# Kernel optimization log

Hardware: AMD Instinct MI355X
Metric: run time of the kernel (lower is better)

## Reference

```python
import jax, jax.numpy as jnp
import numpy as np
from jax import lax

DN = ('NCHW', 'OIHW', 'NCHW')


def setup_inputs() -> dict:
    key = jax.random.key(0)
    ks = jax.random.split(key, 5)
    B, C, H, W = 1, 128, 64, 64
    heads = 4
    return {
        'x_q': jax.random.normal(ks[0], (B, C, H, W), jnp.float32),
        'x_kv': jax.random.normal(ks[1], (B, C, H, W), jnp.float32),
        'w_qkv': jax.random.normal(ks[2], (3 * C, C, 1, 1), jnp.float32) * 0.05,
        'w_dw': jax.random.normal(ks[3], (3 * C, 1, 3, 3), jnp.float32) * 0.2,
        'w_proj': jax.random.normal(ks[4], (C, C, 1, 1), jnp.float32) * 0.05,
        'temperature': jnp.ones((heads, 1, 1), jnp.float32),
    }


def reference(x_q, x_kv, w_qkv, w_dw, w_proj, temperature):
    B, C, H, W = x_q.shape
    heads = temperature.shape[0]
    hd = C // heads
    N = H * W

    # shared qkv 1x1 conv + depthwise 3x3 conv on concatenated [2B,C,H,W]
    x = jnp.concatenate([x_q, x_kv], axis=0)
    qkv = lax.conv_general_dilated(x, w_qkv, (1, 1), 'VALID', dimension_numbers=DN)
    qkv = lax.conv_general_dilated(qkv, w_dw, (1, 1), 'SAME',
                                   feature_group_count=3 * C, dimension_numbers=DN)
    q, k, v = jnp.split(qkv, 3, axis=1)
    q = q[:B]          # query branch from x_q
    k = k[B:]          # key/value branch from x_kv
    v = v[B:]

    def to_heads(t):   # [B,C,H,W] -> [B,h,N,d]
        return t.reshape(B, heads, hd, N).transpose(0, 1, 3, 2)

    attn = jnp.einsum('bhnd,bhmd->bhnm', to_heads(q), to_heads(k)) * temperature
    attn = jax.nn.softmax(attn, axis=-1)
    out = jnp.einsum('bhnm,bhmd->bhnd', attn, to_heads(v))
    out = out.transpose(0, 1, 3, 2).reshape(B, C, H, W)
    return lax.conv_general_dilated(out, w_proj, (1, 1), 'VALID', dimension_numbers=DN)
```

## Files before the change

kernel.cpp:

```cpp
#include <hip/hip_runtime.h>

typedef short bf16x4 __attribute__((ext_vector_type(4)));
typedef short bf16x8 __attribute__((ext_vector_type(8)));
typedef float f32x4 __attribute__((ext_vector_type(4)));
typedef unsigned short u16x4 __attribute__((ext_vector_type(4)));
typedef unsigned short u16x8 __attribute__((ext_vector_type(8)));

__device__ __forceinline__ unsigned short f2bf(float f) {
  union { float f; unsigned u; } v; v.f = f;
  unsigned r = v.u + 0x7FFFu + ((v.u >> 16) & 1u);
  return (unsigned short)(r >> 16);
}
__device__ __forceinline__ unsigned fbits(float f) {
  union { float f; unsigned u; } x; x.f = f; return x.u;
}
__device__ __forceinline__ float bfloat(unsigned u) {
  union { unsigned u; float f; } x; x.u = u; return x.f;
}
__device__ __forceinline__ float fexp2(float x) {
#if __has_builtin(__builtin_amdgcn_exp2f)
  return __builtin_amdgcn_exp2f(x);
#else
  return exp2f(x);
#endif
}
__device__ __forceinline__ f32x4 pv_mfma(bf16x4 a, bf16x4 b, f32x4 c) {
#if __has_builtin(__builtin_amdgcn_mfma_f32_16x16x16bf16_1k)
  return __builtin_amdgcn_mfma_f32_16x16x16bf16_1k(a, b, c, 0, 0, 0);
#else
  bf16x8 az = {a[0], a[1], a[2], a[3], 0, 0, 0, 0};
  bf16x8 bz = {b[0], b[1], b[2], b[3], 0, 0, 0, 0};
  return __builtin_amdgcn_mfma_f32_16x16x32_bf16(az, bz, c, 0, 0, 0);
#endif
}

__global__ __launch_bounds__(256)
void cast_kernel(const float* __restrict__ Xq, const float* __restrict__ Xkv,
                 const float* __restrict__ Wqkv, const float* __restrict__ Wproj,
                 unsigned short* __restrict__ XT, unsigned short* __restrict__ Wq16,
                 unsigned short* __restrict__ Wph, unsigned short* __restrict__ Wpl)
{
  const int b = blockIdx.x, t = threadIdx.x;
  if (b < 256) {
    __shared__ __align__(16) float Tl[64][68];
    const int img = b >> 7, kt = (b >> 6) & 1, nt = b & 63;
    const float* X = img ? Xkv : Xq;
    #pragma unroll
    for (int i = 0; i < 4; ++i) {
      int e = i * 256 + t;
      int r = e >> 4, c4 = (e & 15) * 4;
      *(f32x4*)&Tl[r][c4] = *(const f32x4*)&X[(kt * 64 + r) * 4096 + nt * 64 + c4];
    }
    __syncthreads();
    unsigned short* out = XT + img * (4096 * 128);
    #pragma unroll
    for (int i = 0; i < 2; ++i) {
      int u = i * 256 + t;
      int n = u >> 3, kg = u & 7;
      u16x8 tv;
      #pragma unroll
      for (int j = 0; j < 8; ++j) tv[j] = f2bf(Tl[kg * 8 + j][n]);
      *(u16x8*)&out[(nt * 64 + n) * 128 + kt * 64 + kg * 8] = tv;
    }
  } else {
    const int wb = b - 256;
    if (wb < 3) {
      #pragma unroll 4
      for (int i = 0; i < 64; ++i) {
        int idx = wb * 16384 + i * 256 + t;
        Wq16[idx] = f2bf(Wqkv[idx]);
      }
    } else {
      #pragma unroll 4
      for (int i = 0; i < 64; ++i) {
        int idx = i * 256 + t;
        float v = Wproj[idx];
        unsigned short h = f2bf(v);
        float hf = bfloat((unsigned)h << 16);
        Wph[idx] = h;
        Wpl[idx] = f2bf(v - hf);
      }
    }
  }
}

__global__ __launch_bounds__(256)
void gemm_qkv_kernel(const unsigned short* __restrict__ XT,
                     const unsigned short* __restrict__ Wq16,
                     unsigned short* __restrict__ Y16)
{
  const int t = threadIdx.x;
  const int w = t >> 6, c = t & 15, g = (t & 63) >> 4;
  const int n0 = blockIdx.x * 32;
  const int ob = blockIdx.y;
  const int o_base = ob * 64 + w * 16;
  const unsigned short* B = XT + (ob >= 2 ? 4096 * 128 : 0);
  f32x4 acc0 = {0.f, 0.f, 0.f, 0.f}, acc1 = {0.f, 0.f, 0.f, 0.f};
  #pragma unroll
  for (int ks = 0; ks < 4; ++ks) {
    bf16x8 a = *(const bf16x8*)&Wq16[(o_base + c) * 128 + ks * 32 + g * 8];
    bf16x8 b0 = *(const bf16x8*)&B[(n0 + c) * 128 + ks * 32 + g * 8];
    bf16x8 b1 = *(const bf16x8*)&B[(n0 + 16 + c) * 128 + ks * 32 + g * 8];
    acc0 = __builtin_amdgcn_mfma_f32_16x16x32_bf16(a, b0, acc0, 0, 0, 0);
    acc1 = __builtin_amdgcn_mfma_f32_16x16x32_bf16(a, b1, acc1, 0, 0, 0);
  }
  #pragma unroll
  for (int i = 0; i < 4; ++i) {
    Y16[(o_base + 4 * g + i) * 4096 + n0 + c] = f2bf(acc0[i]);
    Y16[(o_base + 4 * g + i) * 4096 + n0 + 16 + c] = f2bf(acc1[i]);
  }
}

__global__ __launch_bounds__(256)
void gemm_proj_kernel(const unsigned short* __restrict__ Oth,
                      const unsigned short* __restrict__ Otl,
                      const unsigned short* __restrict__ Wph,
                      const unsigned short* __restrict__ Wpl, float* __restrict__ Y)
{
  const int t = threadIdx.x;
  const int w = t >> 6, c = t & 15, g = (t & 63) >> 4;
  const int n0 = blockIdx.x * 32;
  const int o_base = blockIdx.y * 64 + w * 16;
  f32x4 acc0 = {0.f, 0.f, 0.f, 0.f}, acc1 = {0.f, 0.f, 0.f, 0.f};
  #pragma unroll
  for (int ks = 0; ks < 4; ++ks) {
    const int ko = ks * 32 + g * 8;
    bf16x8 ah = *(const bf16x8*)&Wph[(o_base + c) * 128 + ko];
    bf16x8 al = *(const bf16x8*)&Wpl[(o_base + c) * 128 + ko];
    bf16x8 bh0 = *(const bf16x8*)&Oth[(n0 + c) * 128 + ko];
    bf16x8 bl0 = *(const bf16x8*)&Otl[(n0 + c) * 128 + ko];
    bf16x8 bh1 = *(const bf16x8*)&Oth[(n0 + 16 + c) * 128 + ko];
    bf16x8 bl1 = *(const bf16x8*)&Otl[(n0 + 16 + c) * 128 + ko];
    acc0 = __builtin_amdgcn_mfma_f32_16x16x32_bf16(al, bh0, acc0, 0, 0, 0);
    acc0 = __builtin_amdgcn_mfma_f32_16x16x32_bf16(ah, bl0, acc0, 0, 0, 0);
    acc0 = __builtin_amdgcn_mfma_f32_16x16x32_bf16(ah, bh0, acc0, 0, 0, 0);
    acc1 = __builtin_amdgcn_mfma_f32_16x16x32_bf16(al, bh1, acc1, 0, 0, 0);
    acc1 = __builtin_amdgcn_mfma_f32_16x16x32_bf16(ah, bl1, acc1, 0, 0, 0);
    acc1 = __builtin_amdgcn_mfma_f32_16x16x32_bf16(ah, bh1, acc1, 0, 0, 0);
  }
  #pragma unroll
  for (int i = 0; i < 4; ++i) {
    Y[(o_base + 4 * g + i) * 4096 + n0 + c] = acc0[i];
    Y[(o_base + 4 * g + i) * 4096 + n0 + 16 + c] = acc1[i];
  }
}

__global__ __launch_bounds__(256)
void dwconv_kernel(const unsigned short* __restrict__ T16, const float* __restrict__ Wd,
                   const float* __restrict__ temp, unsigned short* __restrict__ Qt,
                   unsigned short* __restrict__ Kt, unsigned short* __restrict__ Vb)
{
  __shared__ __align__(16) float P[4096];
  const int jc = blockIdx.x;
  const int t = threadIdx.x;
  const unsigned short* in = T16 + jc * 4096;
  #pragma unroll
  for (int i = 0; i < 2; ++i) {
    u16x8 v = *(const u16x8*)&in[(i * 256 + t) * 8];
    #pragma unroll
    for (int j = 0; j < 8; ++j)
      P[(i * 256 + t) * 8 + j] = bfloat((unsigned)v[j] << 16);
  }
  float w[9];
  #pragma unroll
  for (int k = 0; k < 9; ++k) w[k] = Wd[jc * 9 + k];
  const float scale = (jc < 128) ? temp[jc >> 5] * 1.4426950408889634f : 1.0f;
  __syncthreads();

  const int hh = (jc >> 5) & 3, dd = jc & 31;
  unsigned short* outT = (jc < 128 ? Qt : Kt) + (hh * 4096) * 32 + dd;
  unsigned short* outV = Vb + (jc - 256) * 4096;
  const bool is_v = (jc >= 256);

  #pragma unroll 4
  for (int i = 0; i < 16; ++i) {
    int idx = i * 256 + t;
    int y = idx >> 6, x = idx & 63;
    float acc = 0.f;
    #pragma unroll
    for (int dy = -1; dy <= 1; ++dy) {
      int yy = y + dy;
      if (yy < 0 || yy > 63) continue;
      #pragma unroll
      for (int dx = -1; dx <= 1; ++dx) {
        int xx = x + dx;
        if (xx < 0 || xx > 63) continue;
        acc += w[(dy + 1) * 3 + (dx + 1)] * P[yy * 64 + xx];
      }
    }
    unsigned short r = f2bf(acc * scale);
    if (is_v) outV[idx] = r;
    else      outT[idx * 32] = r;
  }
}

__global__ __launch_bounds__(1024, 4)
void attn_kernel(const unsigned short* __restrict__ Qt,
                 const unsigned short* __restrict__ Kt,
                 const unsigned short* __restrict__ Vb,
                 unsigned short* __restrict__ Oth, unsigned short* __restrict__ Otl)
{
  __shared__ __align__(16) char lds[40960];
  const int t = threadIdx.x;
  const int wv = t >> 6;
  const int g4 = wv >> 2, qw = wv & 3;
  const int l = t & 63;
  const int c = l & 15, g = l >> 4;
  const int h = blockIdx.y;
  const int nq = blockIdx.x * 64;
  const int m0w = wv * 256;

  bf16x8 qf[4];
  #pragma unroll
  for (int s = 0; s < 4; ++s)
    qf[s] = *(const bf16x8*)&Qt[(h * 4096 + nq + s * 16 + c) * 32 + g * 8];

  f32x4 oh[4][2];
  #pragma unroll
  for (int s = 0; s < 4; ++s) {
    oh[s][0] = (f32x4){0.f, 0.f, 0.f, 0.f};
    oh[s][1] = (f32x4){0.f, 0.f, 0.f, 0.f};
  }
  float lsum[4] = {0.f, 0.f, 0.f, 0.f};

  const unsigned short* Kb  = Kt + (h * 4096 + m0w + c) * 32 + g * 8;
  const unsigned short* Vb0 = Vb + (h * 32 + c) * 4096 + m0w + g * 4;
  const unsigned short* Vb1 = Vb0 + 16 * 4096;

  #pragma unroll 4
  for (int j = 0; j < 16; ++j) {
    bf16x8 kf = *(const bf16x8*)&Kb[j * 512];
    bf16x4 vf0 = *(const bf16x4*)&Vb0[j * 16];
    bf16x4 vf1 = *(const bf16x4*)&Vb1[j * 16];
    #pragma unroll
    for (int s = 0; s < 4; ++s) {
      f32x4 z = {0.f, 0.f, 0.f, 0.f};
      f32x4 sv = __builtin_amdgcn_mfma_f32_16x16x32_bf16(kf, qf[s], z, 0, 0, 0);
      float e0 = fexp2(sv[0]);
      float e1 = fexp2(sv[1]);
      float e2 = fexp2(sv[2]);
      float e3 = fexp2(sv[3]);
      lsum[s] += (e0 + e1) + (e2 + e3);
      union { unsigned u[2]; bf16x4 v; } pu;
      pu.u[0] = __builtin_amdgcn_perm(fbits(e1), fbits(e0), 0x07060302);
      pu.u[1] = __builtin_amdgcn_perm(fbits(e3), fbits(e2), 0x07060302);
      oh[s][0] = pv_mfma(vf0, pu.v, oh[s][0]);
      oh[s][1] = pv_mfma(vf1, pu.v, oh[s][1]);
    }
  }

  #pragma unroll
  for (int s = 0; s < 4; ++s) {
    lsum[s] += __shfl_xor(lsum[s], 16, 64);
    lsum[s] += __shfl_xor(lsum[s], 32, 64);
  }

  __syncthreads();
  float* OG  = (float*)lds;
  float* lfq = (float*)(lds + 34048);
  float* lf  = (float*)(lds + 36864);
  if (l < 16) {
    #pragma unroll
    for (int s = 0; s < 4; ++s)
      lf[(g4 * 4 + qw) * 64 + s * 16 + c] = lsum[s];
  }
  for (int r = 0; r < 4; ++r) {
    if (qw == r) {
      #pragma unroll
      for (int s = 0; s < 4; ++s)
        #pragma unroll
        for (int i = 0; i < 4; ++i) {
          int d0 = 4 * g + i;
          float* p0 = &OG[g4 * 2112 + d0 * 66 + s * 16 + c];
          float* p1 = &OG[g4 * 2112 + (16 + d0) * 66 + s * 16 + c];
          if (r == 0) { *p0 = oh[s][0][i];  *p1 = oh[s][1][i]; }
          else        { *p0 += oh[s][0][i]; *p1 += oh[s][1][i]; }
        }
    }
    __syncthreads();
  }
  if (t < 64) {
    float a = 0.f;
    #pragma unroll
    for (int ww = 0; ww < 16; ++ww) a += lf[ww * 64 + t];
    lfq[t] = a;
  }
  __syncthreads();

  #pragma unroll
  for (int e = t; e < 2048; e += 1024) {
    int d = e & 31, q = e >> 5;
    float s4 = OG[0 * 2112 + d * 66 + q] + OG[1 * 2112 + d * 66 + q] +
               OG[2 * 2112 + d * 66 + q] + OG[3 * 2112 + d * 66 + q];
    float val = s4 / lfq[q];
    unsigned short hi = f2bf(val);
    float hf = bfloat((unsigned)hi << 16);
    int idx = (blockIdx.x * 64 + q) * 128 + h * 32 + d;
    Oth[idx] = hi;
    Otl[idx] = f2bf(val - hf);
  }
}

extern "C" void kernel_launch(void* const* d_in, const int* in_sizes, int n_in,
                              void* d_out, int out_size, void* d_ws, size_t ws_size,
                              hipStream_t stream) {
  const float* xq    = (const float*)d_in[0];
  const float* xkv   = (const float*)d_in[1];
  const float* wqkv  = (const float*)d_in[2];
  const float* wdw   = (const float*)d_in[3];
  const float* wproj = (const float*)d_in[4];
  const float* temp  = (const float*)d_in[5];
  float* out = (float*)d_out;

  char* ws = (char*)d_ws;
  unsigned short* t16  = (unsigned short*)ws;
  unsigned short* xt   = (unsigned short*)(ws + 3145728);
  unsigned short* wq16 = (unsigned short*)(ws + 5242880);
  unsigned short* wph  = (unsigned short*)(ws + 5341184);
  unsigned short* wpl  = (unsigned short*)(ws + 5373952);
  unsigned short* qt   = (unsigned short*)(ws + 5406720);
  unsigned short* kt   = (unsigned short*)(ws + 6455296);
  unsigned short* vb   = (unsigned short*)(ws + 7503872);
  unsigned short* oth  = (unsigned short*)(ws + 8552448);
  unsigned short* otl  = (unsigned short*)(ws + 9601024);

  cast_kernel<<<dim3(260), 256, 0, stream>>>(xq, xkv, wqkv, wproj, xt, wq16, wph, wpl);
  gemm_qkv_kernel<<<dim3(128, 6), 256, 0, stream>>>(xt, wq16, t16);
  dwconv_kernel<<<dim3(384), 256, 0, stream>>>(t16, wdw, temp, qt, kt, vb);
  attn_kernel<<<dim3(64, 4), 1024, 0, stream>>>(qt, kt, vb, oth, otl);
  gemm_proj_kernel<<<dim3(128, 2), 256, 0, stream>>>(oth, otl, wph, wpl, out);
}
```

Measured before the change: 57.38 us.

## Fuse input casting into GEMMs, split dwconv rows, use LDS atomics in attention

Removes the separate cast kernel. The QKV GEMM now reads fp32 inputs and weights directly, transposes through LDS and converts with packed bf16 instructions, while the projection GEMM splits its weights into hi/lo parts on the fly. The depthwise conv is split into four row-quarter blocks per channel with halo loads, which gives more blocks and less LDS each. The attention epilogue replaces the serialized four-round reduction with LDS atomic adds into a single buffer, cutting shared memory and barriers. In exchange it adds redundant weight conversion per block and possible atomic contention in LDS.

Result: slower. 90.80 us (+58.2%).

```diff
diff --git a/kernel.cpp b/kernel.cpp
--- a/kernel.cpp
+++ b/kernel.cpp
@@ -23,6 +23,11 @@
 #else
   return exp2f(x);
 #endif
+}
+__device__ __forceinline__ unsigned cvt_pk_bf16(float a, float b) {
+  unsigned r;
+  asm("v_cvt_pk_bf16_f32 %0, %1, %2" : "=v"(r) : "v"(a), "v"(b));
+  return r;
 }
 __device__ __forceinline__ f32x4 pv_mfma(bf16x4 a, bf16x4 b, f32x4 c) {
 #if __has_builtin(__builtin_amdgcn_mfma_f32_16x16x16bf16_1k)
@@ -35,114 +40,69 @@
 }
 
 __global__ __launch_bounds__(256)
-void cast_kernel(const float* __restrict__ Xq, const float* __restrict__ Xkv,
-                 const float* __restrict__ Wqkv, const float* __restrict__ Wproj,
-                 unsigned short* __restrict__ XT, unsigned short* __restrict__ Wq16,
-                 unsigned short* __restrict__ Wph, unsigned short* __restrict__ Wpl)
+void qkvT_kernel(const float* __restrict__ Xq, const float* __restrict__ Xkv,
+                 const float* __restrict__ Wqkv, unsigned short* __restrict__ Y16)
 {
-  const int b = blockIdx.x, t = threadIdx.x;
-  if (b < 256) {
-    __shared__ __align__(16) float Tl[64][68];
-    const int img = b >> 7, kt = (b >> 6) & 1, nt = b & 63;
-    const float* X = img ? Xkv : Xq;
-    #pragma unroll
-    for (int i = 0; i < 4; ++i) {
-      int e = i * 256 + t;
-      int r = e >> 4, c4 = (e & 15) * 4;
-      *(f32x4*)&Tl[r][c4] = *(const f32x4*)&X[(kt * 64 + r) * 4096 + nt * 64 + c4];
-    }
-    __syncthreads();
-    unsigned short* out = XT + img * (4096 * 128);
-    #pragma unroll
-    for (int i = 0; i < 2; ++i) {
-      int u = i * 256 + t;
-      int n = u >> 3, kg = u & 7;
-      u16x8 tv;
-      #pragma unroll
-      for (int j = 0; j < 8; ++j) tv[j] = f2bf(Tl[kg * 8 + j][n]);
-      *(u16x8*)&out[(nt * 64 + n) * 128 + kt * 64 + kg * 8] = tv;
-    }
-  } else {
-    const int wb = b - 256;
-    if (wb < 3) {
-      #pragma unroll 4
-      for (int i = 0; i < 64; ++i) {
-        int idx = wb * 16384 + i * 256 + t;
-        Wq16[idx] = f2bf(Wqkv[idx]);
-      }
-    } else {
-      #pragma unroll 4
-      for (int i = 0; i < 64; ++i) {
-        int idx = i * 256 + t;
-        float v = Wproj[idx];
-        unsigned short h = f2bf(v);
-        float hf = bfloat((unsigned)h << 16);
-        Wph[idx] = h;
-        Wpl[idx] = f2bf(v - hf);
-      }
-    }
-  }
-}
-
-__global__ __launch_bounds__(256)
-void gemm_qkv_kernel(const unsigned short* __restrict__ XT,
-                     const unsigned short* __restrict__ Wq16,
-                     unsigned short* __restrict__ Y16)
-{
+  __shared__ float Xf[128][33];
   const int t = threadIdx.x;
   const int w = t >> 6, c = t & 15, g = (t & 63) >> 4;
   const int n0 = blockIdx.x * 32;
   const int ob = blockIdx.y;
-  const int o_base = ob * 64 + w * 16;
-  const unsigned short* B = XT + (ob >= 2 ? 4096 * 128 : 0);
-  f32x4 acc0 = {0.f, 0.f, 0.f, 0.f}, acc1 = {0.f, 0.f, 0.f, 0.f};
+  const float* X = (ob >= 2) ? Xkv : Xq;
+
+  {
+    const int kr = t >> 3;
+    const int nc = (t & 7) * 4;
+    #pragma unroll
+    for (int pass = 0; pass < 4; ++pass) {
+      int k = pass * 32 + kr;
+      f32x4 v = *(const f32x4*)&X[k * 4096 + n0 + nc];
+      Xf[k][nc + 0] = v[0];
+      Xf[k][nc + 1] = v[1];
+      Xf[k][nc + 2] = v[2];
+      Xf[k][nc + 3] = v[3];
+    }
+  }
+
+  union { unsigned u[4]; bf16x8 v; } af[4];
+  {
+    const float* wr = Wqkv + (ob * 64 + w * 16 + c) * 128;
+    #pragma unroll
+    for (int ks = 0; ks < 4; ++ks) {
+      f32x4 v0 = *(const f32x4*)&wr[ks * 32 + g * 8];
+      f32x4 v1 = *(const f32x4*)&wr[ks * 32 + g * 8 + 4];
+      af[ks].u[0] = cvt_pk_bf16(v0[0], v0[1]);
+      af[ks].u[1] = cvt_pk_bf16(v0[2], v0[3]);
+      af[ks].u[2] = cvt_pk_bf16(v1[0], v1[1]);
+      af[ks].u[3] = cvt_pk_bf16(v1[2], v1[3]);
+    }
+  }
+  __syncthreads();
+
+  union { unsigned u[4]; bf16x8 v; } bfr[2][4];
+  #pragma unroll
+  for (int s = 0; s < 2; ++s) {
+    const int n = s * 16 + c;
+    #pragma unroll
+    for (int ks = 0; ks < 4; ++ks) {
+      const int kb = ks * 32 + g * 8;
+      #pragma unroll
+      for (int m = 0; m < 4; ++m)
+        bfr[s][ks].u[m] = cvt_pk_bf16(Xf[kb + 2 * m][n], Xf[kb + 2 * m + 1][n]);
+    }
+  }
+
+  f32x4 acc[2] = {{0.f, 0.f, 0.f, 0.f}, {0.f, 0.f, 0.f, 0.f}};
   #pragma unroll
   for (int ks = 0; ks < 4; ++ks) {
-    bf16x8 a = *(const bf16x8*)&Wq16[(o_base + c) * 128 + ks * 32 + g * 8];
-    bf16x8 b0 = *(const bf16x8*)&B[(n0 + c) * 128 + ks * 32 + g * 8];
-    bf16x8 b1 = *(const bf16x8*)&B[(n0 + 16 + c) * 128 + ks * 32 + g * 8];
-    acc0 = __builtin_amdgcn_mfma_f32_16x16x32_bf16(a, b0, acc0, 0, 0, 0);
-    acc1 = __builtin_amdgcn_mfma_f32_16x16x32_bf16(a, b1, acc1, 0, 0, 0);
-  }
-  #pragma unroll
-  for (int i = 0; i < 4; ++i) {
-    Y16[(o_base + 4 * g + i) * 4096 + n0 + c] = f2bf(acc0[i]);
-    Y16[(o_base + 4 * g + i) * 4096 + n0 + 16 + c] = f2bf(acc1[i]);
-  }
-}
-
-__global__ __launch_bounds__(256)
-void gemm_proj_kernel(const unsigned short* __restrict__ Oth,
-                      const unsigned short* __restrict__ Otl,
-                      const unsigned short* __restrict__ Wph,
-                      const unsigned short* __restrict__ Wpl, float* __restrict__ Y)
-{
-  const int t = threadIdx.x;
-  const int w = t >> 6, c = t & 15, g = (t & 63) >> 4;
-  const int n0 = blockIdx.x * 32;
-  const int o_base = blockIdx.y * 64 + w * 16;
-  f32x4 acc0 = {0.f, 0.f, 0.f, 0.f}, acc1 = {0.f, 0.f, 0.f, 0.f};
-  #pragma unroll
-  for (int ks = 0; ks < 4; ++ks) {
-    const int ko = ks * 32 + g * 8;
-    bf16x8 ah = *(const bf16x8*)&Wph[(o_base + c) * 128 + ko];
-    bf16x8 al = *(const bf16x8*)&Wpl[(o_base + c) * 128 + ko];
-    bf16x8 bh0 = *(const bf16x8*)&Oth[(n0 + c) * 128 + ko];
-    bf16x8 bl0 = *(const bf16x8*)&Otl[(n0 + c) * 128 + ko];
-    bf16x8 bh1 = *(const bf16x8*)&Oth[(n0 + 16 + c) * 128 + ko];
-    bf16x8 bl1 = *(const bf16x8*)&Otl[(n0 + 16 + c) * 128 + ko];
-    acc0 = __builtin_amdgcn_mfma_f32_16x16x32_bf16(al, bh0, acc0, 0, 0, 0);
-    acc0 = __builtin_amdgcn_mfma_f32_16x16x32_bf16(ah, bl0, acc0, 0, 0, 0);
-    acc0 = __builtin_amdgcn_mfma_f32_16x16x32_bf16(ah, bh0, acc0, 0, 0, 0);
-    acc1 = __builtin_amdgcn_mfma_f32_16x16x32_bf16(al, bh1, acc1, 0, 0, 0);
-    acc1 = __builtin_amdgcn_mfma_f32_16x16x32_bf16(ah, bl1, acc1, 0, 0, 0);
-    acc1 = __builtin_amdgcn_mfma_f32_16x16x32_bf16(ah, bh1, acc1, 0, 0, 0);
-  }
-  #pragma unroll
-  for (int i = 0; i < 4; ++i) {
-    Y[(o_base + 4 * g + i) * 4096 + n0 + c] = acc0[i];
-    Y[(o_base + 4 * g + i) * 4096 + n0 + 16 + c] = acc1[i];
-  }
+    acc[0] = __builtin_amdgcn_mfma_f32_16x16x32_bf16(af[ks].v, bfr[0][ks].v, acc[0], 0, 0, 0);
+    acc[1] = __builtin_amdgcn_mfma_f32_16x16x32_bf16(af[ks].v, bfr[1][ks].v, acc[1], 0, 0, 0);
+  }
+  #pragma unroll
+  for (int s = 0; s < 2; ++s)
+    #pragma unroll
+    for (int i = 0; i < 4; ++i)
+      Y16[(ob * 64 + w * 16 + 4 * g + i) * 4096 + n0 + s * 16 + c] = f2bf(acc[s][i]);
 }
 
 __global__ __launch_bounds__(256)
@@ -150,16 +110,20 @@
                    const float* __restrict__ temp, unsigned short* __restrict__ Qt,
                    unsigned short* __restrict__ Kt, unsigned short* __restrict__ Vb)
 {
-  __shared__ __align__(16) float P[4096];
-  const int jc = blockIdx.x;
+  __shared__ float P[18 * 64];
+  const int jc = blockIdx.x >> 2;
+  const int qtr = blockIdx.x & 3;
+  const int y0 = qtr * 16;
   const int t = threadIdx.x;
   const unsigned short* in = T16 + jc * 4096;
   #pragma unroll
-  for (int i = 0; i < 2; ++i) {
-    u16x8 v = *(const u16x8*)&in[(i * 256 + t) * 8];
-    #pragma unroll
-    for (int j = 0; j < 8; ++j)
-      P[(i * 256 + t) * 8 + j] = bfloat((unsigned)v[j] << 16);
+  for (int i = 0; i < 5; ++i) {
+    int idx = i * 256 + t;
+    if (idx < 1152) {
+      int row = idx >> 6, col = idx & 63;
+      int sy = y0 - 1 + row;
+      P[idx] = (sy >= 0 && sy < 64) ? bfloat((unsigned)in[sy * 64 + col] << 16) : 0.f;
+    }
   }
   float w[9];
   #pragma unroll
@@ -168,29 +132,25 @@
   __syncthreads();
 
   const int hh = (jc >> 5) & 3, dd = jc & 31;
-  unsigned short* outT = (jc < 128 ? Qt : Kt) + (hh * 4096) * 32 + dd;
-  unsigned short* outV = Vb + (jc - 256) * 4096;
+  unsigned short* outT = (jc < 128 ? Qt : Kt) + hh * 4096 * 32 + dd;
+  unsigned short* outV = Vb + (jc - 256) * 4096 + y0 * 64;
   const bool is_v = (jc >= 256);
 
-  #pragma unroll 4
-  for (int i = 0; i < 16; ++i) {
-    int idx = i * 256 + t;
-    int y = idx >> 6, x = idx & 63;
+  #pragma unroll
+  for (int i = 0; i < 4; ++i) {
+    int p = i * 256 + t;
+    int yl = p >> 6, x = p & 63;
     float acc = 0.f;
     #pragma unroll
-    for (int dy = -1; dy <= 1; ++dy) {
-      int yy = y + dy;
-      if (yy < 0 || yy > 63) continue;
-      #pragma unroll
-      for (int dx = -1; dx <= 1; ++dx) {
-        int xx = x + dx;
-        if (xx < 0 || xx > 63) continue;
-        acc += w[(dy + 1) * 3 + (dx + 1)] * P[yy * 64 + xx];
-      }
+    for (int dy = 0; dy < 3; ++dy) {
+      int base = (yl + dy) * 64 + x;
+      if (x > 0)  acc += w[dy * 3 + 0] * P[base - 1];
+      acc += w[dy * 3 + 1] * P[base];
+      if (x < 63) acc += w[dy * 3 + 2] * P[base + 1];
     }
     unsigned short r = f2bf(acc * scale);
-    if (is_v) outV[idx] = r;
-    else      outT[idx * 32] = r;
+    if (is_v) outV[p] = r;
+    else      outT[(y0 * 64 + p) * 32] = r;
   }
 }
 
@@ -200,10 +160,9 @@
                  const unsigned short* __restrict__ Vb,
                  unsigned short* __restrict__ Oth, unsigned short* __restrict__ Otl)
 {
-  __shared__ __align__(16) char lds[40960];
+  __shared__ __align__(16) char lds[12544];
   const int t = threadIdx.x;
   const int wv = t >> 6;
-  const int g4 = wv >> 2, qw = wv & 3;
   const int l = t & 63;
   const int c = l & 15, g = l >> 4;
   const int h = blockIdx.y;
@@ -255,49 +214,83 @@
     lsum[s] += __shfl_xor(lsum[s], 32, 64);
   }
 
+  float* OG = (float*)lds;
+  float* lf = (float*)(lds + 8448);
+  #pragma unroll
+  for (int e = t; e < 2112; e += 1024) OG[e] = 0.f;
+  if (l < 16) {
+    #pragma unroll
+    for (int s = 0; s < 4; ++s)
+      lf[wv * 64 + s * 16 + c] = lsum[s];
+  }
   __syncthreads();
-  float* OG  = (float*)lds;
-  float* lfq = (float*)(lds + 34048);
-  float* lf  = (float*)(lds + 36864);
-  if (l < 16) {
-    #pragma unroll
-    for (int s = 0; s < 4; ++s)
-      lf[(g4 * 4 + qw) * 64 + s * 16 + c] = lsum[s];
-  }
-  for (int r = 0; r < 4; ++r) {
-    if (qw == r) {
-      #pragma unroll
-      for (int s = 0; s < 4; ++s)
-        #pragma unroll
-        for (int i = 0; i < 4; ++i) {
-          int d0 = 4 * g + i;
-          float* p0 = &OG[g4 * 2112 + d0 * 66 + s * 16 + c];
-          float* p1 = &OG[g4 * 2112 + (16 + d0) * 66 + s * 16 + c];
-          if (r == 0) { *p0 = oh[s][0][i];  *p1 = oh[s][1][i]; }
-          else        { *p0 += oh[s][0][i]; *p1 += oh[s][1][i]; }
-        }
-    }
-    __syncthreads();
-  }
-  if (t < 64) {
-    float a = 0.f;
-    #pragma unroll
-    for (int ww = 0; ww < 16; ++ww) a += lf[ww * 64 + t];
-    lfq[t] = a;
-  }
+  #pragma unroll
+  for (int s = 0; s < 4; ++s)
+    #pragma unroll
+    for (int i = 0; i < 4; ++i) {
+      int d0 = 4 * g + i;
+      unsafeAtomicAdd(&OG[d0 * 66 + s * 16 + c], oh[s][0][i]);
+      unsafeAtomicAdd(&OG[(16 + d0) * 66 + s * 16 + c], oh[s][1][i]);
+    }
   __syncthreads();
 
   #pragma unroll
   for (int e = t; e < 2048; e += 1024) {
     int d = e & 31, q = e >> 5;
-    float s4 = OG[0 * 2112 + d * 66 + q] + OG[1 * 2112 + d * 66 + q] +
-               OG[2 * 2112 + d * 66 + q] + OG[3 * 2112 + d * 66 + q];
-    float val = s4 / lfq[q];
+    float li = 0.f;
+    #pragma unroll
+    for (int ww = 0; ww < 16; ++ww) li += lf[ww * 64 + q];
+    float val = OG[d * 66 + q] / li;
     unsigned short hi = f2bf(val);
     float hf = bfloat((unsigned)hi << 16);
     int idx = (blockIdx.x * 64 + q) * 128 + h * 32 + d;
     Oth[idx] = hi;
     Otl[idx] = f2bf(val - hf);
+  }
+}
+
+__global__ __launch_bounds__(256)
+void gemm_proj_kernel(const unsigned short* __restrict__ Oth,
+                      const unsigned short* __restrict__ Otl,
+                      const float* __restrict__ Wp, float* __restrict__ Y)
+{
+  const int t = threadIdx.x;
+  const int w = t >> 6, c = t & 15, g = (t & 63) >> 4;
+  const int n0 = blockIdx.x * 32;
+  const int o_base = blockIdx.y * 64 + w * 16;
+  f32x4 acc0 = {0.f, 0.f, 0.f, 0.f}, acc1 = {0.f, 0.f, 0.f, 0.f};
+  #pragma unroll
+  for (int ks = 0; ks < 4; ++ks) {
+    const int ko = ks * 32 + g * 8;
+    const float* wr = Wp + (o_base + c) * 128 + ko;
+    union { unsigned u[4]; bf16x8 v; } ah, al;
+    #pragma unroll
+    for (int m = 0; m < 2; ++m) {
+      f32x4 v = *(const f32x4*)&wr[m * 4];
+      #pragma unroll
+      for (int p = 0; p < 2; ++p) {
+        unsigned hw = cvt_pk_bf16(v[2 * p], v[2 * p + 1]);
+        float h0 = bfloat(hw << 16);
+        float h1 = bfloat(hw & 0xFFFF0000u);
+        ah.u[m * 2 + p] = hw;
+        al.u[m * 2 + p] = cvt_pk_bf16(v[2 * p] - h0, v[2 * p + 1] - h1);
+      }
+    }
+    bf16x8 bh0 = *(const bf16x8*)&Oth[(n0 + c) * 128 + ko];
+    bf16x8 bl0 = *(const bf16x8*)&Otl[(n0 + c) * 128 + ko];
+    bf16x8 bh1 = *(const bf16x8*)&Oth[(n0 + 16 + c) * 128 + ko];
+    bf16x8 bl1 = *(const bf16x8*)&Otl[(n0 + 16 + c) * 128 + ko];
+    acc0 = __builtin_amdgcn_mfma_f32_16x16x32_bf16(al.v, bh0, acc0, 0, 0, 0);
+    acc0 = __builtin_amdgcn_mfma_f32_16x16x32_bf16(ah.v, bl0, acc0, 0, 0, 0);
+    acc0 = __builtin_amdgcn_mfma_f32_16x16x32_bf16(ah.v, bh0, acc0, 0, 0, 0);
+    acc1 = __builtin_amdgcn_mfma_f32_16x16x32_bf16(al.v, bh1, acc1, 0, 0, 0);
+    acc1 = __builtin_amdgcn_mfma_f32_16x16x32_bf16(ah.v, bl1, acc1, 0, 0, 0);
+    acc1 = __builtin_amdgcn_mfma_f32_16x16x32_bf16(ah.v, bh1, acc1, 0, 0, 0);
+  }
+  #pragma unroll
+  for (int i = 0; i < 4; ++i) {
+    Y[(o_base + 4 * g + i) * 4096 + n0 + c] = acc0[i];
+    Y[(o_base + 4 * g + i) * 4096 + n0 + 16 + c] = acc1[i];
   }
 }
 
@@ -313,20 +306,15 @@
   float* out = (float*)d_out;
 
   char* ws = (char*)d_ws;
-  unsigned short* t16  = (unsigned short*)ws;
-  unsigned short* xt   = (unsigned short*)(ws + 3145728);
-  unsigned short* wq16 = (unsigned short*)(ws + 5242880);
-  unsigned short* wph  = (unsigned short*)(ws + 5341184);
-  unsigned short* wpl  = (unsigned short*)(ws + 5373952);
-  unsigned short* qt   = (unsigned short*)(ws + 5406720);
-  unsigned short* kt   = (unsigned short*)(ws + 6455296);
-  unsigned short* vb   = (unsigned short*)(ws + 7503872);
-  unsigned short* oth  = (unsigned short*)(ws + 8552448);
-  unsigned short* otl  = (unsigned short*)(ws + 9601024);
-
-  cast_kernel<<<dim3(260), 256, 0, stream>>>(xq, xkv, wqkv, wproj, xt, wq16, wph, wpl);
-  gemm_qkv_kernel<<<dim3(128, 6), 256, 0, stream>>>(xt, wq16, t16);
-  dwconv_kernel<<<dim3(384), 256, 0, stream>>>(t16, wdw, temp, qt, kt, vb);
+  unsigned short* t16 = (unsigned short*)ws;
+  unsigned short* qt  = (unsigned short*)(ws + 3145728);
+  unsigned short* kt  = (unsigned short*)(ws + 4194304);
+  unsigned short* vb  = (unsigned short*)(ws + 5242880);
+  unsigned short* oth = (unsigned short*)(ws + 6291456);
+  unsigned short* otl = (unsigned short*)(ws + 7340032);
+
+  qkvT_kernel<<<dim3(128, 6), 256, 0, stream>>>(xq, xkv, wqkv, t16);
+  dwconv_kernel<<<dim3(1536), 256, 0, stream>>>(t16, wdw, temp, qt, kt, vb);
   attn_kernel<<<dim3(64, 4), 1024, 0, stream>>>(qt, kt, vb, oth, otl);
-  gemm_proj_kernel<<<dim3(128, 2), 256, 0, stream>>>(oth, otl, wph, wpl, out);
-}
+  gemm_proj_kernel<<<dim3(128, 2), 256, 0, stream>>>(oth, otl, wproj, out);
+}
```
